# Kernel tuning notes

Measured on AMD Instinct MI355X. Metric: run time of the kernel, lower is better.

## Reference

```python
import jax, jax.numpy as jnp
import numpy as np
from jax import lax

HIDDEN = 2048
INTER = 4096          # mamba_expand * hidden_size
HEADS = 64
HEAD_DIM = 64         # HEADS * HEAD_DIM == INTER
STATE = 64
GROUPS = 1
KCONV = 4
CONV_DIM = INTER + 2 * GROUPS * STATE   # 4224
PROJ = INTER + CONV_DIM + HEADS          # 8384
SSM_IN_MULT = 1.0
Z_MULT, X_MULT, B_MULT, C_MULT, DT_MULT = 1.0, 1.0, 1.0, 1.0, 1.0
EPS = 1e-6


def setup_inputs() -> dict:
    key = jax.random.key(0)
    ks = jax.random.split(key, 4)
    B, L = 1, 2048
    return {
        "hidden_states": jax.random.normal(ks[0], (B, L, HIDDEN), jnp.float32),
        "in_proj_w": jax.random.normal(ks[1], (PROJ, HIDDEN), jnp.float32) / np.sqrt(HIDDEN),
        "conv_w": jax.random.normal(ks[2], (CONV_DIM, KCONV), jnp.float32) / np.sqrt(KCONV),
        "conv_b": jnp.zeros((CONV_DIM,), jnp.float32),
        "dt_bias": jnp.ones((HEADS,), jnp.float32),
        "A_log": jnp.log(jnp.arange(1, HEADS + 1, dtype=jnp.float32)),
        "D": jnp.ones((HEADS,), jnp.float32),
        "norm_weight": jnp.ones((INTER,), jnp.float32),
        "out_proj_w": jax.random.normal(ks[3], (HIDDEN, INTER), jnp.float32) / np.sqrt(INTER),
    }


def reference(hidden_states, in_proj_w, conv_w, conv_b, dt_bias, A_log, D,
              norm_weight, out_proj_w):
    Bsz, L, _ = hidden_states.shape
    gns = GROUPS * STATE

    # ----- in_proj + per-split multipliers -----
    proj = (hidden_states * SSM_IN_MULT) @ in_proj_w.T          # [B,L,PROJ]
    gate = proj[..., :INTER] * Z_MULT                           # z
    hBC = proj[..., INTER:INTER + CONV_DIM]
    dt = proj[..., INTER + CONV_DIM:] * DT_MULT                 # [B,L,H]
    hBC = jnp.concatenate(
        [hBC[..., :INTER] * X_MULT,
         hBC[..., INTER:INTER + gns] * B_MULT,
         hBC[..., INTER + gns:] * C_MULT], axis=-1)

    # ----- causal depthwise conv1d (left pad K-1, truncate to L) + SiLU -----
    padded = jnp.pad(hBC, ((0, 0), (KCONV - 1, 0), (0, 0)))
    conv = conv_b
    for k in range(KCONV):
        conv = conv + padded[:, k:k + L, :] * conv_w[:, k]
    hBC = jax.nn.silu(conv)

    x = hBC[..., :INTER].reshape(Bsz, L, HEADS, HEAD_DIM)       # [B,L,H,P]
    Bm = hBC[..., INTER:INTER + gns].reshape(Bsz, L, GROUPS, STATE)
    Cm = hBC[..., INTER + gns:].reshape(Bsz, L, GROUPS, STATE)
    hpg = HEADS // GROUPS
    B_h = jnp.repeat(Bm, hpg, axis=2)                           # [B,L,H,N]
    C_h = jnp.repeat(Cm, hpg, axis=2)

    # ----- selective SSM recurrence -----
    dt = jax.nn.softplus(dt + dt_bias)                          # [B,L,H] (>0; clamp(0,inf) no-op)
    A = -jnp.exp(A_log)                                         # [H]
    dA = jnp.exp(dt * A)                                        # [B,L,H]
    dtx = dt[..., None] * x                                     # [B,L,H,P]

    def step(s, inp):
        dA_t, dtx_t, B_t, C_t = inp                             # [B,H], [B,H,P], [B,H,N], [B,H,N]
        s = dA_t[..., None, None] * s + dtx_t[..., None] * B_t[:, :, None, :]
        y_t = jnp.einsum('bhpn,bhn->bhp', s, C_t)
        return s, y_t

    tm = lambda a: jnp.moveaxis(a, 1, 0)  # time-major
    s0 = jnp.zeros((Bsz, HEADS, HEAD_DIM, STATE), jnp.float32)
    _, ys = lax.scan(step, s0, (tm(dA), tm(dtx), tm(B_h), tm(C_h)))
    y = jnp.moveaxis(ys, 0, 1) + D[None, None, :, None] * x     # [B,L,H,P]
    y = y.reshape(Bsz, L, INTER)

    # ----- gated RMSNorm (norm before gate) -----
    yg = y.reshape(Bsz, L, GROUPS, INTER // GROUPS)
    var = jnp.mean(yg * yg, axis=-1, keepdims=True)
    yg = yg * lax.rsqrt(var + EPS) * norm_weight.reshape(GROUPS, INTER // GROUPS)
    y = yg.reshape(Bsz, L, INTER) * jax.nn.silu(gate)

    return y @ out_proj_w.T                                     # [B,L,HIDDEN]
```

## Files before the change

### kernel.cpp

```cpp
#include <hip/hip_runtime.h>
#include <hip/hip_bf16.h>
#include <cstdint>
#include <cstddef>

#define SEQLEN   2048
#define HIDDEN   2048
#define INTER    4096
#define NHEADS   64
#define NSTATE   64
#define CONVD    4224
#define LDPROJ   8448
#define NCHUNK   32
#define CHUNK    64

typedef __attribute__((ext_vector_type(8))) short bf16x8_t;
typedef __attribute__((ext_vector_type(4))) float f32x4_t;

__device__ __forceinline__ void cp16(void* lds, const void* g) {
    __builtin_amdgcn_global_load_lds(
        (const __attribute__((address_space(1))) unsigned int*)g,
        (__attribute__((address_space(3))) unsigned int*)lds, 16, 0, 0);
}

__global__ void k_split(const float* __restrict__ in, unsigned short* __restrict__ hi,
                        unsigned short* __restrict__ lo, long nvalid, long ntotal) {
    long i = (long)blockIdx.x * 256 + threadIdx.x;
    if (i >= ntotal) return;
    float x = (i < nvalid) ? in[i] : 0.0f;
    __hip_bfloat16 h = __float2bfloat16(x);
    float hf = __bfloat162float(h);
    __hip_bfloat16 l = __float2bfloat16(x - hf);
    hi[i] = *reinterpret_cast<unsigned short*>(&h);
    lo[i] = *reinterpret_cast<unsigned short*>(&l);
}

__global__ void k_split_hi(const float* __restrict__ in, unsigned short* __restrict__ hi,
                           long nvalid, long ntotal) {
    long i = (long)blockIdx.x * 256 + threadIdx.x;
    if (i >= ntotal) return;
    float x = (i < nvalid) ? in[i] : 0.0f;
    __hip_bfloat16 h = __float2bfloat16(x);
    hi[i] = *reinterpret_cast<unsigned short*>(&h);
}

__global__ void k_split_lo(const float* __restrict__ in, unsigned short* __restrict__ lo,
                           long nvalid, long ntotal) {
    long i = (long)blockIdx.x * 256 + threadIdx.x;
    if (i >= ntotal) return;
    float x = (i < nvalid) ? in[i] : 0.0f;
    __hip_bfloat16 h = __float2bfloat16(x);
    float hf = __bfloat162float(h);
    __hip_bfloat16 l = __float2bfloat16(x - hf);
    lo[i] = *reinterpret_cast<unsigned short*>(&l);
}

__global__ __launch_bounds__(256, 2)
void k_gemm_split(const unsigned short* __restrict__ Ah, const unsigned short* __restrict__ Al,
                  const unsigned short* __restrict__ Bh, const unsigned short* __restrict__ Bl,
                  float* __restrict__ C, int K, int ldc,
                  int mb_count, int strip_w, int split_col) {
    __shared__ unsigned short sA[2][2][4096];
    __shared__ unsigned short sB[2][2][4096];

    const int tid  = threadIdx.x;
    const int lane = tid & 63;
    const int w    = tid >> 6;
    const int wm   = w >> 1, wn = w & 1;

    const int span   = mb_count * strip_w;
    const int strip  = blockIdx.x / span;
    const int within = blockIdx.x % span;
    const int mblk = within % mb_count;
    const int nblk = strip * strip_w + within / mb_count;
    const long bm  = (long)mblk * 128;
    const long bn  = (long)nblk * 128;
    const bool do_lo = (bn >= (long)split_col);

    f32x4_t acc[4][4];
#pragma unroll
    for (int i = 0; i < 4; ++i)
#pragma unroll
        for (int j = 0; j < 4; ++j) acc[i][j] = (f32x4_t){0.f, 0.f, 0.f, 0.f};

    const int srow = lane & 15;
    const int c8   = (lane >> 4) << 3;

    auto stage = [&](int k0, int buf) {
#pragma unroll
        for (int j = 0; j < 2; ++j) {
            const int chunk = j * 4 + w;
            const int r     = chunk * 16 + srow;
            const long gA   = (bm + r) * (long)K + k0 + c8;
            const long gB   = (bn + r) * (long)K + k0 + c8;
            const int lbase = chunk * 512;
            cp16(&sA[buf][0][lbase], Ah + gA);
            cp16(&sB[buf][0][lbase], Bh + gB);
            if (do_lo) {
                cp16(&sA[buf][1][lbase], Al + gA);
                cp16(&sB[buf][1][lbase], Bl + gB);
            }
        }
    };

    const int NK = K >> 5;
    stage(0, 0);

    for (int it = 0; it < NK; ++it) {
        const int cur = it & 1;
        __syncthreads();

        bf16x8_t fah[4], fbh[4], fal[4], fbl[4];
#pragma unroll
        for (int mi = 0; mi < 4; ++mi)
            fah[mi] = *(const bf16x8_t*)&sA[cur][0][(wm * 4 + mi) * 512 + lane * 8];
#pragma unroll
        for (int ni = 0; ni < 4; ++ni)
            fbh[ni] = *(const bf16x8_t*)&sB[cur][0][(wn * 4 + ni) * 512 + lane * 8];
        if (do_lo) {
#pragma unroll
            for (int mi = 0; mi < 4; ++mi)
                fal[mi] = *(const bf16x8_t*)&sA[cur][1][(wm * 4 + mi) * 512 + lane * 8];
#pragma unroll
            for (int ni = 0; ni < 4; ++ni)
                fbl[ni] = *(const bf16x8_t*)&sB[cur][1][(wn * 4 + ni) * 512 + lane * 8];
        }

        if (it + 1 < NK) stage((it + 1) << 5, cur ^ 1);

        if (do_lo) {
#pragma unroll
            for (int mi = 0; mi < 4; ++mi)
#pragma unroll
                for (int ni = 0; ni < 4; ++ni) {
                    acc[mi][ni] = __builtin_amdgcn_mfma_f32_16x16x32_bf16(fah[mi], fbh[ni], acc[mi][ni], 0, 0, 0);
                    acc[mi][ni] = __builtin_amdgcn_mfma_f32_16x16x32_bf16(fah[mi], fbl[ni], acc[mi][ni], 0, 0, 0);
                    acc[mi][ni] = __builtin_amdgcn_mfma_f32_16x16x32_bf16(fal[mi], fbh[ni], acc[mi][ni], 0, 0, 0);
                }
        } else {
#pragma unroll
            for (int mi = 0; mi < 4; ++mi)
#pragma unroll
                for (int ni = 0; ni < 4; ++ni)
                    acc[mi][ni] = __builtin_amdgcn_mfma_f32_16x16x32_bf16(fah[mi], fbh[ni], acc[mi][ni], 0, 0, 0);
        }
    }

    const int col = lane & 15;
    const int rq  = (lane >> 4) << 2;
#pragma unroll
    for (int mi = 0; mi < 4; ++mi)
#pragma unroll
        for (int ni = 0; ni < 4; ++ni) {
            long mb_ = bm + wm * 64 + mi * 16 + rq;
            long nb_ = bn + wn * 64 + ni * 16 + col;
#pragma unroll
            for (int r = 0; r < 4; ++r) C[(mb_ + r) * (long)ldc + nb_] = acc[mi][ni][r];
        }
}

__global__ __launch_bounds__(256)
void k_conv(const float* __restrict__ proj, const float* __restrict__ cw,
            const float* __restrict__ cb, float* __restrict__ xbc) {
    int c  = blockIdx.x * 256 + threadIdx.x;
    int t0 = blockIdx.y * 8;
    if (c >= CONVD) return;
    const float cw0 = cw[c * 4], cw1 = cw[c * 4 + 1], cw2 = cw[c * 4 + 2], cw3 = cw[c * 4 + 3];
    const float b = cb[c];
    float h[11];
#pragma unroll
    for (int i = 0; i < 11; ++i) {
        int tt = t0 - 3 + i;
        h[i] = (tt >= 0) ? proj[(size_t)tt * LDPROJ + INTER + c] : 0.f;
    }
#pragma unroll
    for (int k = 0; k < 8; ++k) {
        float acc = b + h[k] * cw0 + h[k + 1] * cw1 + h[k + 2] * cw2 + h[k + 3] * cw3;
        float s = acc / (1.f + expf(-acc));
        xbc[(size_t)(t0 + k) * CONVD + c] = s;
    }
}

__global__ __launch_bounds__(256)
void k_cum(const float* __restrict__ proj, const float* __restrict__ dtb,
           float* __restrict__ dt, float* __restrict__ cd) {
    const int tid  = threadIdx.x;
    const int lane = tid & 63;
    const int wid  = blockIdx.x * 4 + (tid >> 6);
    const int c    = wid >> 6;
    const int h    = wid & 63;
    const int t    = c * CHUNK + lane;
    float raw = proj[(size_t)t * LDPROJ + 8320 + h] + dtb[h];
    float sp  = (raw > 20.f) ? raw : log1pf(expf(raw));
    float x = sp;
#pragma unroll
    for (int off = 1; off < 64; off <<= 1) {
        float v = __shfl_up(x, off, 64);
        if (lane >= off) x += v;
    }
    dt[t * 64 + h] = sp;
    cd[t * 64 + h] = x;
}

__global__ __launch_bounds__(256, 2)
void k_ssdA(const float* __restrict__ xbc, const float* __restrict__ dt,
            const float* __restrict__ cd, const float* __restrict__ alog,
            const float* __restrict__ Dp, float* __restrict__ y,
            float* __restrict__ M) {
    __shared__ float Xs[64][68];
    __shared__ float Bs[64][68];
    __shared__ float Cs[64][68];
    __shared__ float dts[64], cds[64], wts[64];
    float (*Gs)[68] = Cs;

    const int c = blockIdx.x, h = blockIdx.y;
    const int tid = threadIdx.x;
    const int tr = tid >> 4, tc = tid & 15;
    const int t0 = c * CHUNK;
    const float A = -__expf(alog[h]);

    for (int i = tid; i < 4096; i += 256) {
        int t = i >> 6, j = i & 63;
        size_t base = (size_t)(t0 + t) * CONVD;
        Xs[t][j] = xbc[base + h * 64 + j];
        Bs[t][j] = xbc[base + INTER + j];
        Cs[t][j] = xbc[base + INTER + 64 + j];
    }
    if (tid < 64) {
        dts[tid] = dt[(t0 + tid) * 64 + h];
        cds[tid] = cd[(t0 + tid) * 64 + h];
    }
    __syncthreads();
    if (tid < 64) wts[tid] = __expf(A * (cds[63] - cds[tid])) * dts[tid];

    float g[4][4];
#pragma unroll
    for (int i = 0; i < 4; ++i)
#pragma unroll
        for (int j = 0; j < 4; ++j) g[i][j] = 0.f;
    for (int n = 0; n < 64; n += 4) {
        float4 cv[4], bv[4];
#pragma unroll
        for (int i = 0; i < 4; ++i) cv[i] = *(const float4*)&Cs[tr * 4 + i][n];
#pragma unroll
        for (int j = 0; j < 4; ++j) bv[j] = *(const float4*)&Bs[tc * 4 + j][n];
#pragma unroll
        for (int i = 0; i < 4; ++i)
#pragma unroll
            for (int j = 0; j < 4; ++j)
                g[i][j] += cv[i].x * bv[j].x + cv[i].y * bv[j].y +
                           cv[i].z * bv[j].z + cv[i].w * bv[j].w;
    }
    __syncthreads();
#pragma unroll
    for (int i = 0; i < 4; ++i) {
        int t = tr * 4 + i;
#pragma unroll
        for (int j = 0; j < 4; ++j) {
            int tau = tc * 4 + j;
            float v = (tau <= t) ? g[i][j] * __expf(A * (cds[t] - cds[tau])) * dts[tau] : 0.f;
            Gs[t][tau] = v;
        }
    }
    __syncthreads();

    float accY[4][4], accM[4][4];
#pragma unroll
    for (int i = 0; i < 4; ++i)
#pragma unroll
        for (int j = 0; j < 4; ++j) { accY[i][j] = 0.f; accM[i][j] = 0.f; }

    for (int tau = 0; tau < 64; tau += 4) {
        float4 gv[4], xv[4];
#pragma unroll
        for (int i = 0; i < 4; ++i) gv[i] = *(const float4*)&Gs[tr * 4 + i][tau];
#pragma unroll
        for (int k = 0; k < 4; ++k) xv[k] = *(const float4*)&Xs[tau + k][tc * 4];
#pragma unroll
        for (int i = 0; i < 4; ++i) {
            accY[i][0] += gv[i].x * xv[0].x + gv[i].y * xv[1].x + gv[i].z * xv[2].x + gv[i].w * xv[3].x;
            accY[i][1] += gv[i].x * xv[0].y + gv[i].y * xv[1].y + gv[i].z * xv[2].y + gv[i].w * xv[3].y;
            accY[i][2] += gv[i].x * xv[0].z + gv[i].y * xv[1].z + gv[i].z * xv[2].z + gv[i].w * xv[3].z;
            accY[i][3] += gv[i].x * xv[0].w + gv[i].y * xv[1].w + gv[i].z * xv[2].w + gv[i].w * xv[3].w;
        }
#pragma unroll
        for (int k = 0; k < 4; ++k) {
            float wv = wts[tau + k];
            float4 bv = *(const float4*)&Bs[tau + k][tr * 4];
            float4 xk = xv[k];
            float wb0 = wv * bv.x, wb1 = wv * bv.y, wb2 = wv * bv.z, wb3 = wv * bv.w;
            accM[0][0] += wb0 * xk.x; accM[0][1] += wb0 * xk.y; accM[0][2] += wb0 * xk.z; accM[0][3] += wb0 * xk.w;
            accM[1][0] += wb1 * xk.x; accM[1][1] += wb1 * xk.y; accM[1][2] += wb1 * xk.z; accM[1][3] += wb1 * xk.w;
            accM[2][0] += wb2 * xk.x; accM[2][1] += wb2 * xk.y; accM[2][2] += wb2 * xk.z; accM[2][3] += wb2 * xk.w;
            accM[3][0] += wb3 * xk.x; accM[3][1] += wb3 * xk.y; accM[3][2] += wb3 * xk.z; accM[3][3] += wb3 * xk.w;
        }
    }

    const float Dv = Dp[h];
#pragma unroll
    for (int i = 0; i < 4; ++i) {
        int t = tr * 4 + i;
        float4 o;
        o.x = accY[i][0] + Dv * Xs[t][tc * 4 + 0];
        o.y = accY[i][1] + Dv * Xs[t][tc * 4 + 1];
        o.z = accY[i][2] + Dv * Xs[t][tc * 4 + 2];
        o.w = accY[i][3] + Dv * Xs[t][tc * 4 + 3];
        *(float4*)&y[(size_t)(t0 + t) * INTER + h * 64 + tc * 4] = o;
    }
    size_t mbase = ((size_t)(c * 64 + h)) << 12;
#pragma unroll
    for (int i = 0; i < 4; ++i) {
        float4 o = { accM[i][0], accM[i][1], accM[i][2], accM[i][3] };
        *(float4*)&M[mbase + (size_t)(tr * 4 + i) * 64 + tc * 4] = o;
    }
}

__global__ __launch_bounds__(256)
void k_state(const float* __restrict__ M, const float* __restrict__ cd,
             const float* __restrict__ alog, float* __restrict__ Sprev) {
    const int g  = blockIdx.x * 256 + threadIdx.x;
    const int h  = g >> 12;
    const int np = g & 4095;
    const float A = -__expf(alog[h]);
    float s = 0.f;
#pragma unroll 1
    for (int c = 0; c < NCHUNK; ++c) {
        size_t idx = (((size_t)(c * 64 + h)) << 12) + np;
        Sprev[idx] = s;
        float decay = __expf(A * cd[((c * CHUNK + 63) * 64) + h]);
        s = decay * s + M[idx];
    }
}

__global__ __launch_bounds__(256, 2)
void k_ssdC(const float* __restrict__ xbc, const float* __restrict__ cd,
            const float* __restrict__ alog, const float* __restrict__ Sprev,
            float* __restrict__ y) {
    __shared__ float Ss[64][68];
    __shared__ float Cs[64][68];
    __shared__ float cds[64];
    const int c = blockIdx.x, h = blockIdx.y;
    const int tid = threadIdx.x;
    const int tr = tid >> 4, tc = tid & 15;
    const int t0 = c * CHUNK;
    const float A = -__expf(alog[h]);

    size_t sbase = ((size_t)(c * 64 + h)) << 12;
    for (int i = tid; i < 4096; i += 256) {
        int n = i >> 6, p = i & 63;
        Ss[n][p] = Sprev[sbase + i];
        Cs[n][p] = xbc[(size_t)(t0 + n) * CONVD + INTER + 64 + p];
    }
    if (tid < 64) cds[tid] = cd[(t0 + tid) * 64 + h];
    __syncthreads();

    float acc[4][4];
#pragma unroll
    for (int i = 0; i < 4; ++i)
#pragma unroll
        for (int j = 0; j < 4; ++j) acc[i][j] = 0.f;

    for (int n = 0; n < 64; n += 4) {
        float4 cv[4], sv[4];
#pragma unroll
        for (int i = 0; i < 4; ++i) cv[i] = *(const float4*)&Cs[tr * 4 + i][n];
#pragma unroll
        for (int k = 0; k < 4; ++k) sv[k] = *(const float4*)&Ss[n + k][tc * 4];
#pragma unroll
        for (int i = 0; i < 4; ++i) {
            acc[i][0] += cv[i].x * sv[0].x + cv[i].y * sv[1].x + cv[i].z * sv[2].x + cv[i].w * sv[3].x;
            acc[i][1] += cv[i].x * sv[0].y + cv[i].y * sv[1].y + cv[i].z * sv[2].y + cv[i].w * sv[3].y;
            acc[i][2] += cv[i].x * sv[0].z + cv[i].y * sv[1].z + cv[i].z * sv[2].z + cv[i].w * sv[3].z;
            acc[i][3] += cv[i].x * sv[0].w + cv[i].y * sv[1].w + cv[i].z * sv[2].w + cv[i].w * sv[3].w;
        }
    }

#pragma unroll
    for (int i = 0; i < 4; ++i) {
        int t = tr * 4 + i;
        float sc = __expf(A * cds[t]);
        size_t yi = (size_t)(t0 + t) * INTER + h * 64 + tc * 4;
        float4 cur = *(const float4*)&y[yi];
        cur.x += sc * acc[i][0];
        cur.y += sc * acc[i][1];
        cur.z += sc * acc[i][2];
        cur.w += sc * acc[i][3];
        *(float4*)&y[yi] = cur;
    }
}

__global__ __launch_bounds__(256)
void k_norm(const float* __restrict__ y, const float* __restrict__ proj,
            const float* __restrict__ nw, unsigned short* __restrict__ ygh,
            unsigned short* __restrict__ ygl) {
    __shared__ float red[4];
    const int t = blockIdx.x, tid = threadIdx.x;
    float sum = 0.f;
    for (int i = tid; i < INTER; i += 256) {
        float v = y[(size_t)t * INTER + i];
        sum += v * v;
    }
#pragma unroll
    for (int off = 32; off >= 1; off >>= 1) sum += __shfl_xor(sum, off, 64);
    if ((tid & 63) == 0) red[tid >> 6] = sum;
    __syncthreads();
    float var = (red[0] + red[1] + red[2] + red[3]) * (1.f / INTER);
    float rs  = rsqrtf(var + 1e-6f);
    for (int i = tid; i < INTER; i += 256) {
        float v = y[(size_t)t * INTER + i] * rs * nw[i];
        float g = proj[(size_t)t * LDPROJ + i];
        float o = v * (g / (1.f + expf(-g)));
        __hip_bfloat16 hh = __float2bfloat16(o);
        float hf = __bfloat162float(hh);
        __hip_bfloat16 ll = __float2bfloat16(o - hf);
        ygh[(size_t)t * INTER + i] = *reinterpret_cast<unsigned short*>(&hh);
        ygl[(size_t)t * INTER + i] = *reinterpret_cast<unsigned short*>(&ll);
    }
}

#define OFF_HSHI  ((size_t)0)
#define OFF_HSLO  ((size_t)8388608)
#define OFF_YGH   ((size_t)0)
#define OFF_W1HI  ((size_t)16777216)
#define OFF_W1LO  ((size_t)(16777216 + 34603008))
#define OFF_M     ((size_t)16777216)
#define OFF_SPREV ((size_t)50331648)
#define OFF_W2HI  ((size_t)16777216)
#define OFF_W2LO  ((size_t)33554432)
#define OFF_PROJ  ((size_t)85983232)
#define OFF_XBC   ((size_t)155189248)
#define OFF_DT    ((size_t)189792256)
#define OFF_CD    ((size_t)190316544)
#define OFF_Y     ((size_t)190840832)
#define OFF_YGL   ((size_t)224395264)

extern "C" void kernel_launch(void* const* d_in, const int* in_sizes, int n_in,
                              void* d_out, int out_size, void* d_ws, size_t ws_size,
                              hipStream_t stream) {
    (void)in_sizes; (void)n_in; (void)out_size; (void)ws_size;
    const float* hs   = (const float*)d_in[0];
    const float* w1   = (const float*)d_in[1];
    const float* cw   = (const float*)d_in[2];
    const float* cb   = (const float*)d_in[3];
    const float* dtb  = (const float*)d_in[4];
    const float* alog = (const float*)d_in[5];
    const float* Dp   = (const float*)d_in[6];
    const float* nw   = (const float*)d_in[7];
    const float* w2   = (const float*)d_in[8];
    float* out = (float*)d_out;
    char* ws = (char*)d_ws;

    unsigned short* hs_hi = (unsigned short*)(ws + OFF_HSHI);
    unsigned short* hs_lo = (unsigned short*)(ws + OFF_HSLO);
    unsigned short* w1_hi = (unsigned short*)(ws + OFF_W1HI);
    unsigned short* w1_lo = (unsigned short*)(ws + OFF_W1LO);
    unsigned short* w2_hi = (unsigned short*)(ws + OFF_W2HI);
    unsigned short* w2_lo = (unsigned short*)(ws + OFF_W2LO);
    unsigned short* ygh   = (unsigned short*)(ws + OFF_YGH);
    unsigned short* ygl   = (unsigned short*)(ws + OFF_YGL);
    float* proj  = (float*)(ws + OFF_PROJ);
    float* xbc   = (float*)(ws + OFF_XBC);
    float* dtv   = (float*)(ws + OFF_DT);
    float* cdv   = (float*)(ws + OFF_CD);
    float* y     = (float*)(ws + OFF_Y);
    float* M     = (float*)(ws + OFF_M);
    float* Sprev = (float*)(ws + OFF_SPREV);

    k_split<<<16384, 256, 0, stream>>>(hs, hs_hi, hs_lo, 4194304L, 4194304L);
    k_split_hi<<<67584, 256, 0, stream>>>(w1, w1_hi, 17170432L, 17301504L);
    k_split_lo<<<2048, 256, 0, stream>>>(w1 + (size_t)8192 * 2048, w1_lo, 393216L, 524288L);

    const unsigned short* w1_lo_base = w1_lo - (size_t)8192 * 2048;
    k_gemm_split<<<1056, 256, 0, stream>>>(hs_hi, hs_lo, w1_hi, w1_lo_base, proj,
                                           HIDDEN, LDPROJ, 16, 6, 8192);

    k_conv<<<dim3(17, 256), 256, 0, stream>>>(proj, cw, cb, xbc);
    k_cum<<<512, 256, 0, stream>>>(proj, dtb, dtv, cdv);

    k_ssdA<<<dim3(NCHUNK, NHEADS), 256, 0, stream>>>(xbc, dtv, cdv, alog, Dp, y, M);
    k_state<<<1024, 256, 0, stream>>>(M, cdv, alog, Sprev);
    k_ssdC<<<dim3(NCHUNK, NHEADS), 256, 0, stream>>>(xbc, cdv, alog, Sprev, y);

    k_norm<<<SEQLEN, 256, 0, stream>>>(y, proj, nw, ygh, ygl);

    k_split<<<32768, 256, 0, stream>>>(w2, w2_hi, w2_lo, 8388608L, 8388608L);

    k_gemm_split<<<256, 256, 0, stream>>>(ygh, ygl, w2_hi, w2_lo, out,
                                          INTER, HIDDEN, 16, 4, 0);
}
```

Before: 685.6 us.

## Split GEMMs into bf16-only and split-precision kernels; use split-K for out_proj

The in_proj GEMM now runs a dedicated bf16-only kernel (higher occupancy, smaller LDS) for the gate/x columns. A small split-precision kernel handles only the B/C/dt column tail with hi/lo corrections. The out_proj GEMM drops its lo terms entirely, so the norm output and w2 are no longer split into hi and lo parts, and it uses a 4-way split-K with atomicAdd into a zeroed output to raise parallelism. This removes the extra MFMAs and conversion traffic at the cost of lower precision on out_proj and atomic nondeterminism.

```diff
diff --git a/kernel.cpp b/kernel.cpp
--- a/kernel.cpp
+++ b/kernel.cpp
@@ -54,13 +54,11 @@
     lo[i] = *reinterpret_cast<unsigned short*>(&l);
 }
 
-__global__ __launch_bounds__(256, 2)
-void k_gemm_split(const unsigned short* __restrict__ Ah, const unsigned short* __restrict__ Al,
-                  const unsigned short* __restrict__ Bh, const unsigned short* __restrict__ Bl,
-                  float* __restrict__ C, int K, int ldc,
-                  int mb_count, int strip_w, int split_col) {
-    __shared__ unsigned short sA[2][2][4096];
-    __shared__ unsigned short sB[2][2][4096];
+__global__ __launch_bounds__(256, 4)
+void k_gemm_hi(const unsigned short* __restrict__ Ah, const unsigned short* __restrict__ Bh,
+               float* __restrict__ C, int K, int ldc, int mb_count, int strip_w) {
+    __shared__ unsigned short sA[2][4096];
+    __shared__ unsigned short sB[2][4096];
 
     const int tid  = threadIdx.x;
     const int lane = tid & 63;
@@ -74,7 +72,100 @@
     const int nblk = strip * strip_w + within / mb_count;
     const long bm  = (long)mblk * 128;
     const long bn  = (long)nblk * 128;
-    const bool do_lo = (bn >= (long)split_col);
+
+    const int KS    = gridDim.y;
+    const int Kc    = K / KS;
+    const int kbase = blockIdx.y * Kc;
+
+    f32x4_t acc[4][4];
+#pragma unroll
+    for (int i = 0; i < 4; ++i)
+#pragma unroll
+        for (int j = 0; j < 4; ++j) acc[i][j] = (f32x4_t){0.f, 0.f, 0.f, 0.f};
+
+    const int srow = lane & 15;
+    const int c8   = (lane >> 4) << 3;
+
+    auto stage = [&](int k0, int buf) {
+#pragma unroll
+        for (int j = 0; j < 2; ++j) {
+            const int chunk = j * 4 + w;
+            const int r     = chunk * 16 + srow;
+            const long gA   = (bm + r) * (long)K + k0 + c8;
+            const long gB   = (bn + r) * (long)K + k0 + c8;
+            const int lbase = chunk * 512;
+            cp16(&sA[buf][lbase], Ah + gA);
+            cp16(&sB[buf][lbase], Bh + gB);
+        }
+    };
+
+    const int NK = Kc >> 5;
+    stage(kbase, 0);
+
+    for (int it = 0; it < NK; ++it) {
+        const int cur = it & 1;
+        __syncthreads();
+
+        bf16x8_t fah[4], fbh[4];
+#pragma unroll
+        for (int mi = 0; mi < 4; ++mi)
+            fah[mi] = *(const bf16x8_t*)&sA[cur][(wm * 4 + mi) * 512 + lane * 8];
+#pragma unroll
+        for (int ni = 0; ni < 4; ++ni)
+            fbh[ni] = *(const bf16x8_t*)&sB[cur][(wn * 4 + ni) * 512 + lane * 8];
+
+        if (it + 1 < NK) stage(kbase + ((it + 1) << 5), cur ^ 1);
+
+#pragma unroll
+        for (int mi = 0; mi < 4; ++mi)
+#pragma unroll
+            for (int ni = 0; ni < 4; ++ni)
+                acc[mi][ni] = __builtin_amdgcn_mfma_f32_16x16x32_bf16(fah[mi], fbh[ni], acc[mi][ni], 0, 0, 0);
+    }
+
+    const int col = lane & 15;
+    const int rq  = (lane >> 4) << 2;
+    if (KS > 1) {
+#pragma unroll
+        for (int mi = 0; mi < 4; ++mi)
+#pragma unroll
+            for (int ni = 0; ni < 4; ++ni) {
+                long mb_ = bm + wm * 64 + mi * 16 + rq;
+                long nb_ = bn + wn * 64 + ni * 16 + col;
+#pragma unroll
+                for (int r = 0; r < 4; ++r)
+                    atomicAdd(&C[(mb_ + r) * (long)ldc + nb_], acc[mi][ni][r]);
+            }
+    } else {
+#pragma unroll
+        for (int mi = 0; mi < 4; ++mi)
+#pragma unroll
+            for (int ni = 0; ni < 4; ++ni) {
+                long mb_ = bm + wm * 64 + mi * 16 + rq;
+                long nb_ = bn + wn * 64 + ni * 16 + col;
+#pragma unroll
+                for (int r = 0; r < 4; ++r) C[(mb_ + r) * (long)ldc + nb_] = acc[mi][ni][r];
+            }
+    }
+}
+
+__global__ __launch_bounds__(256, 2)
+void k_gemm_split(const unsigned short* __restrict__ Ah, const unsigned short* __restrict__ Al,
+                  const unsigned short* __restrict__ Bh, const unsigned short* __restrict__ Bl,
+                  float* __restrict__ C, int K, int ldc,
+                  int mb_count, int nbase) {
+    __shared__ unsigned short sA[2][2][4096];
+    __shared__ unsigned short sB[2][2][4096];
+
+    const int tid  = threadIdx.x;
+    const int lane = tid & 63;
+    const int w    = tid >> 6;
+    const int wm   = w >> 1, wn = w & 1;
+
+    const int mblk = blockIdx.x % mb_count;
+    const int nblk = blockIdx.x / mb_count;
+    const long bm  = (long)mblk * 128;
+    const long bn  = (long)nbase + (long)nblk * 128;
 
     f32x4_t acc[4][4];
 #pragma unroll
@@ -95,10 +186,8 @@
             const int lbase = chunk * 512;
             cp16(&sA[buf][0][lbase], Ah + gA);
             cp16(&sB[buf][0][lbase], Bh + gB);
-            if (do_lo) {
-                cp16(&sA[buf][1][lbase], Al + gA);
-                cp16(&sB[buf][1][lbase], Bl + gB);
-            }
+            cp16(&sA[buf][1][lbase], Al + gA);
+            cp16(&sB[buf][1][lbase], Bl + gB);
         }
     };
 
@@ -111,38 +200,26 @@
 
         bf16x8_t fah[4], fbh[4], fal[4], fbl[4];
 #pragma unroll
+        for (int mi = 0; mi < 4; ++mi) {
+            fah[mi] = *(const bf16x8_t*)&sA[cur][0][(wm * 4 + mi) * 512 + lane * 8];
+            fal[mi] = *(const bf16x8_t*)&sA[cur][1][(wm * 4 + mi) * 512 + lane * 8];
+        }
+#pragma unroll
+        for (int ni = 0; ni < 4; ++ni) {
+            fbh[ni] = *(const bf16x8_t*)&sB[cur][0][(wn * 4 + ni) * 512 + lane * 8];
+            fbl[ni] = *(const bf16x8_t*)&sB[cur][1][(wn * 4 + ni) * 512 + lane * 8];
+        }
+
+        if (it + 1 < NK) stage((it + 1) << 5, cur ^ 1);
+
+#pragma unroll
         for (int mi = 0; mi < 4; ++mi)
-            fah[mi] = *(const bf16x8_t*)&sA[cur][0][(wm * 4 + mi) * 512 + lane * 8];
-#pragma unroll
-        for (int ni = 0; ni < 4; ++ni)
-            fbh[ni] = *(const bf16x8_t*)&sB[cur][0][(wn * 4 + ni) * 512 + lane * 8];
-        if (do_lo) {
-#pragma unroll
-            for (int mi = 0; mi < 4; ++mi)
-                fal[mi] = *(const bf16x8_t*)&sA[cur][1][(wm * 4 + mi) * 512 + lane * 8];
-#pragma unroll
-            for (int ni = 0; ni < 4; ++ni)
-                fbl[ni] = *(const bf16x8_t*)&sB[cur][1][(wn * 4 + ni) * 512 + lane * 8];
-        }
-
-        if (it + 1 < NK) stage((it + 1) << 5, cur ^ 1);
-
-        if (do_lo) {
-#pragma unroll
-            for (int mi = 0; mi < 4; ++mi)
-#pragma unroll
-                for (int ni = 0; ni < 4; ++ni) {
-                    acc[mi][ni] = __builtin_amdgcn_mfma_f32_16x16x32_bf16(fah[mi], fbh[ni], acc[mi][ni], 0, 0, 0);
-                    acc[mi][ni] = __builtin_amdgcn_mfma_f32_16x16x32_bf16(fah[mi], fbl[ni], acc[mi][ni], 0, 0, 0);
-                    acc[mi][ni] = __builtin_amdgcn_mfma_f32_16x16x32_bf16(fal[mi], fbh[ni], acc[mi][ni], 0, 0, 0);
-                }
-        } else {
-#pragma unroll
-            for (int mi = 0; mi < 4; ++mi)
-#pragma unroll
-                for (int ni = 0; ni < 4; ++ni)
-                    acc[mi][ni] = __builtin_amdgcn_mfma_f32_16x16x32_bf16(fah[mi], fbh[ni], acc[mi][ni], 0, 0, 0);
-        }
+#pragma unroll
+            for (int ni = 0; ni < 4; ++ni) {
+                acc[mi][ni] = __builtin_amdgcn_mfma_f32_16x16x32_bf16(fah[mi], fbh[ni], acc[mi][ni], 0, 0, 0);
+                acc[mi][ni] = __builtin_amdgcn_mfma_f32_16x16x32_bf16(fah[mi], fbl[ni], acc[mi][ni], 0, 0, 0);
+                acc[mi][ni] = __builtin_amdgcn_mfma_f32_16x16x32_bf16(fal[mi], fbh[ni], acc[mi][ni], 0, 0, 0);
+            }
     }
 
     const int col = lane & 15;
@@ -390,8 +467,7 @@
 
 __global__ __launch_bounds__(256)
 void k_norm(const float* __restrict__ y, const float* __restrict__ proj,
-            const float* __restrict__ nw, unsigned short* __restrict__ ygh,
-            unsigned short* __restrict__ ygl) {
+            const float* __restrict__ nw, unsigned short* __restrict__ ygh) {
     __shared__ float red[4];
     const int t = blockIdx.x, tid = threadIdx.x;
     float sum = 0.f;
@@ -410,28 +486,23 @@
         float g = proj[(size_t)t * LDPROJ + i];
         float o = v * (g / (1.f + expf(-g)));
         __hip_bfloat16 hh = __float2bfloat16(o);
-        float hf = __bfloat162float(hh);
-        __hip_bfloat16 ll = __float2bfloat16(o - hf);
         ygh[(size_t)t * INTER + i] = *reinterpret_cast<unsigned short*>(&hh);
-        ygl[(size_t)t * INTER + i] = *reinterpret_cast<unsigned short*>(&ll);
     }
 }
 
 #define OFF_HSHI  ((size_t)0)
 #define OFF_HSLO  ((size_t)8388608)
-#define OFF_YGH   ((size_t)0)
-#define OFF_W1HI  ((size_t)16777216)
-#define OFF_W1LO  ((size_t)(16777216 + 34603008))
-#define OFF_M     ((size_t)16777216)
-#define OFF_SPREV ((size_t)50331648)
-#define OFF_W2HI  ((size_t)16777216)
-#define OFF_W2LO  ((size_t)33554432)
-#define OFF_PROJ  ((size_t)85983232)
-#define OFF_XBC   ((size_t)155189248)
-#define OFF_DT    ((size_t)189792256)
-#define OFF_CD    ((size_t)190316544)
-#define OFF_Y     ((size_t)190840832)
-#define OFF_YGL   ((size_t)224395264)
+#define OFF_YGH   ((size_t)16777216)
+#define OFF_W1HI  ((size_t)33554432)
+#define OFF_M     ((size_t)33554432)
+#define OFF_W1LO  ((size_t)68157440)
+#define OFF_SPREV ((size_t)69206016)
+#define OFF_PROJ  ((size_t)102760448)
+#define OFF_XBC   ((size_t)171966464)
+#define OFF_DT    ((size_t)206569472)
+#define OFF_CD    ((size_t)207093760)
+#define OFF_Y     ((size_t)207618048)
+#define OFF_W2HI  ((size_t)207618048)
 
 extern "C" void kernel_launch(void* const* d_in, const int* in_sizes, int n_in,
                               void* d_out, int out_size, void* d_ws, size_t ws_size,
@@ -454,9 +525,7 @@
     unsigned short* w1_hi = (unsigned short*)(ws + OFF_W1HI);
     unsigned short* w1_lo = (unsigned short*)(ws + OFF_W1LO);
     unsigned short* w2_hi = (unsigned short*)(ws + OFF_W2HI);
-    unsigned short* w2_lo = (unsigned short*)(ws + OFF_W2LO);
     unsigned short* ygh   = (unsigned short*)(ws + OFF_YGH);
-    unsigned short* ygl   = (unsigned short*)(ws + OFF_YGL);
     float* proj  = (float*)(ws + OFF_PROJ);
     float* xbc   = (float*)(ws + OFF_XBC);
     float* dtv   = (float*)(ws + OFF_DT);
@@ -469,9 +538,10 @@
     k_split_hi<<<67584, 256, 0, stream>>>(w1, w1_hi, 17170432L, 17301504L);
     k_split_lo<<<2048, 256, 0, stream>>>(w1 + (size_t)8192 * 2048, w1_lo, 393216L, 524288L);
 
+    k_gemm_hi<<<dim3(1024, 1), 256, 0, stream>>>(hs_hi, w1_hi, proj, HIDDEN, LDPROJ, 16, 8);
     const unsigned short* w1_lo_base = w1_lo - (size_t)8192 * 2048;
-    k_gemm_split<<<1056, 256, 0, stream>>>(hs_hi, hs_lo, w1_hi, w1_lo_base, proj,
-                                           HIDDEN, LDPROJ, 16, 6, 8192);
+    k_gemm_split<<<32, 256, 0, stream>>>(hs_hi, hs_lo, w1_hi, w1_lo_base, proj,
+                                         HIDDEN, LDPROJ, 16, 8192);
 
     k_conv<<<dim3(17, 256), 256, 0, stream>>>(proj, cw, cb, xbc);
     k_cum<<<512, 256, 0, stream>>>(proj, dtb, dtv, cdv);
@@ -480,10 +550,10 @@
     k_state<<<1024, 256, 0, stream>>>(M, cdv, alog, Sprev);
     k_ssdC<<<dim3(NCHUNK, NHEADS), 256, 0, stream>>>(xbc, cdv, alog, Sprev, y);
 
-    k_norm<<<SEQLEN, 256, 0, stream>>>(y, proj, nw, ygh, ygl);
-
-    k_split<<<32768, 256, 0, stream>>>(w2, w2_hi, w2_lo, 8388608L, 8388608L);
-
-    k_gemm_split<<<256, 256, 0, stream>>>(ygh, ygl, w2_hi, w2_lo, out,
-                                          INTER, HIDDEN, 16, 4, 0);
-}
+    k_norm<<<SEQLEN, 256, 0, stream>>>(y, proj, nw, ygh);
+
+    k_split_hi<<<32768, 256, 0, stream>>>(w2, w2_hi, 8388608L, 8388608L);
+
+    hipMemsetAsync(out, 0, (size_t)SEQLEN * HIDDEN * sizeof(float), stream);
+    k_gemm_hi<<<dim3(256, 4), 256, 0, stream>>>(ygh, w2_hi, out, INTER, HIDDEN, 16, 16);
+}
```

Result: faster. 632.5 us (-7.8%).
